# Performance work log

Hardware: AMD Instinct MI355X
Metric: run time of the kernel (lower is better)

## Reference

```python
import jax, jax.numpy as jnp
import numpy as np

B, S, H = 4, 2048, 1024

def setup_inputs() -> dict:
    key = jax.random.key(0)
    ks = jax.random.split(key, 6)
    scale = 1.0 / np.sqrt(H)
    return {
        "query": jax.random.normal(ks[0], (B, S, H), dtype=jnp.float32),
        "key":   jax.random.normal(ks[1], (B, S, H), dtype=jnp.float32),
        "value": jax.random.normal(ks[2], (B, S, H), dtype=jnp.float32),
        "Wq": jax.random.normal(ks[3], (H, H), dtype=jnp.float32) * scale,
        "Wk": jax.random.normal(ks[4], (H, H), dtype=jnp.float32) * scale,
        "Wv": jax.random.normal(ks[5], (H, H), dtype=jnp.float32) * scale,
    }

def reference(query, key, value, Wq, Wk, Wv):
    # nn.Linear(bias=False): y = x @ W.T
    q = jnp.einsum('bsh,oh->bso', query, Wq)
    k = jnp.einsum('bsh,oh->bso', key, Wk)
    v = jnp.einsum('bsh,oh->bso', value, Wv)
    # full QK^T scores [B, Q, K], scaled by sqrt(hidden_size)
    scores = jnp.einsum('bqh,bkh->bqk', q, k) / jnp.sqrt(jnp.asarray(H, q.dtype))
    attn = jax.nn.softmax(scores, axis=2)
    return jnp.einsum('bqk,bkh->bqh', attn, v)
```

## Files before the change

### kernel.cpp

```cpp
#include <hip/hip_runtime.h>
#include <hip/hip_bf16.h>
#include <stdint.h>

#define BATCH 4
#define SLEN  2048
#define HID   1024

typedef __attribute__((ext_vector_type(8))) short bfrag8;
typedef __attribute__((ext_vector_type(4))) float facc4;
typedef __attribute__((ext_vector_type(4))) unsigned short us4;

__device__ __forceinline__ unsigned short f2b(float f) {
  union { float f; unsigned int i; } x; x.f = f;
  unsigned int r = x.i + 0x7FFFu + ((x.i >> 16) & 1u);
  return (unsigned short)(r >> 16);
}

__device__ __forceinline__ void gl_lds16(const void* g, void* l) {
  __builtin_amdgcn_global_load_lds(
      (const __attribute__((address_space(1))) void*)g,
      (__attribute__((address_space(3))) void*)l, 16, 0, 0);
}

__global__ __launch_bounds__(256) void cast_all(
    const float* __restrict__ q, const float* __restrict__ k,
    const float* __restrict__ v, const float* __restrict__ wq,
    const float* __restrict__ wk, const float* __restrict__ wv,
    us4* __restrict__ dst, float* __restrict__ lsum) {
  if (blockIdx.x < 8) {
    float4 z = {0.f, 0.f, 0.f, 0.f};
    ((float4*)lsum)[blockIdx.x * 256 + threadIdx.x] = z;
  }
  const long i = (long)blockIdx.x * 256 + threadIdx.x;
  const long S1 = 2097152, S2 = 4194304, S3 = 6291456,
             S4 = 6553600, S5 = 6815744;
  const float4* src; long off;
  if (i < S2) {
    if (i < S1) { src = (const float4*)q;  off = i; }
    else        { src = (const float4*)k;  off = i - S1; }
  } else if (i < S3) { src = (const float4*)v;  off = i - S2; }
  else if   (i < S4) { src = (const float4*)wq; off = i - S3; }
  else if   (i < S5) { src = (const float4*)wk; off = i - S4; }
  else               { src = (const float4*)wv; off = i - S5; }
  float4 x = src[off];
  us4 o;
  o.x = f2b(x.x); o.y = f2b(x.y); o.z = f2b(x.z); o.w = f2b(x.w);
  dst[i] = o;
}

template <int NT>
__device__ __forceinline__ void core256(
    const unsigned short* __restrict__ A, const unsigned short* __restrict__ B,
    const int lda, const int ldb,
    unsigned short* __restrict__ As, unsigned short* __restrict__ Bs,
    facc4 (&acc)[8][4]) {
  const int tid  = threadIdx.x;
  const int lane = tid & 63;
  const int wave = tid >> 6;
  const int wm = wave >> 2;
  const int wn = wave & 3;
  const int ln = lane & 15;
  const int lq = lane >> 4;
  const int swz = ln & 7;

  const int row0 = tid >> 3;
  const int blk  = (tid & 7) ^ (row0 & 7);
  const unsigned short* pA = A + (long)row0 * lda + blk * 8;
  const unsigned short* pB = B + (long)row0 * ldb + blk * 8;
  const long a64 = 64l * lda, b64 = 64l * ldb;
  unsigned short* dA = As + tid * 8;
  unsigned short* dB = Bs + tid * 8;

#define STG_A(h, b, t) do { const unsigned short* g_ = pA + (h) * (a64 * 2) + (long)(t) * 64; \
    gl_lds16(g_,       dA + (b) * 16384 + (h) * 8192); \
    gl_lds16(g_ + a64, dA + (b) * 16384 + (h) * 8192 + 4096); } while (0)
#define STG_B(h, b, t) do { const unsigned short* g_ = pB + (h) * (b64 * 2) + (long)(t) * 64; \
    gl_lds16(g_,       dB + (b) * 16384 + (h) * 8192); \
    gl_lds16(g_ + b64, dB + (b) * 16384 + (h) * 8192 + 4096); } while (0)

  const int o0 = (lq ^ swz) * 8;
  const int o1 = ((4 + lq) ^ swz) * 8;
  const int aOfs = wm * 8192 + ln * 64;
  const int bOfs = (wn >> 1) * 8192 + ((wn & 1) * 64 + ln) * 64;

#define RD_A4(dst, bufb, mb) do { \
  _Pragma("unroll") for (int m_ = 0; m_ < 4; ++m_) { \
    dst[m_][0] = *(const bfrag8*)(As + (bufb) + aOfs + ((mb) + m_) * 1024 + o0); \
    dst[m_][1] = *(const bfrag8*)(As + (bufb) + aOfs + ((mb) + m_) * 1024 + o1); \
  } } while (0)
#define RD_B2(dst, bufb, nb) do { \
  _Pragma("unroll") for (int n_ = 0; n_ < 2; ++n_) { \
    dst[n_][0] = *(const bfrag8*)(Bs + (bufb) + bOfs + ((nb) + n_) * 1024 + o0); \
    dst[n_][1] = *(const bfrag8*)(Bs + (bufb) + bOfs + ((nb) + n_) * 1024 + o1); \
  } } while (0)

#define MFMAQ(AF, BF, MO, NO) do { \
  _Pragma("unroll") for (int m_ = 0; m_ < 4; ++m_) \
  _Pragma("unroll") for (int n_ = 0; n_ < 2; ++n_) { \
    acc[(MO)+m_][(NO)+n_] = __builtin_amdgcn_mfma_f32_16x16x32_bf16( \
        AF[m_][0], BF[n_][0], acc[(MO)+m_][(NO)+n_], 0, 0, 0); \
    acc[(MO)+m_][(NO)+n_] = __builtin_amdgcn_mfma_f32_16x16x32_bf16( \
        AF[m_][1], BF[n_][1], acc[(MO)+m_][(NO)+n_], 0, 0, 0); \
  } } while (0)

  bfrag8 a0[4][2], a1[4][2], b0[2][2], b1[2][2], a0n[4][2], b0n[2][2];

  STG_B(0, 0, 0); STG_A(0, 0, 0); STG_A(1, 0, 0); STG_B(1, 0, 0);
  STG_B(0, 1, 1); STG_A(0, 1, 1); STG_A(1, 1, 1); STG_B(1, 1, 1);
  asm volatile("s_waitcnt vmcnt(8)" ::: "memory");
  __builtin_amdgcn_s_barrier();
  RD_A4(a0, 0, 0);
  RD_B2(b0, 0, 0);

#pragma unroll
  for (int t = 0; t < NT; ++t) {
    const int bb = (t & 1) * 16384;
    const int nb = bb ^ 16384;

    RD_B2(b1, bb, 2);
    __builtin_amdgcn_s_setprio(1);
    MFMAQ(a0, b0, 0, 0);
    __builtin_amdgcn_s_setprio(0);
    __builtin_amdgcn_s_barrier();

    RD_A4(a1, bb, 4);
    if (t + 2 < NT) STG_B(0, t & 1, t + 2);
    __builtin_amdgcn_s_setprio(1);
    MFMAQ(a0, b1, 0, 2);
    __builtin_amdgcn_s_setprio(0);
    if (t + 2 < NT) asm volatile("s_waitcnt vmcnt(2)" ::: "memory");
    else            asm volatile("s_waitcnt vmcnt(0)" ::: "memory");
    __builtin_amdgcn_s_barrier();

    if (t + 1 < NT) RD_A4(a0n, nb, 0);
    if (t + 2 < NT) STG_A(0, t & 1, t + 2);
    __builtin_amdgcn_s_setprio(1);
    MFMAQ(a1, b1, 4, 2);
    __builtin_amdgcn_s_setprio(0);

    if (t + 1 < NT) RD_B2(b0n, nb, 0);
    if (t + 2 < NT) { STG_A(1, t & 1, t + 2); STG_B(1, t & 1, t + 2); }
    __builtin_amdgcn_s_setprio(1);
    MFMAQ(a1, b0, 4, 0);
    __builtin_amdgcn_s_setprio(0);
    __builtin_amdgcn_s_barrier();

    if (t + 1 < NT) {
#pragma unroll
      for (int m_ = 0; m_ < 4; ++m_) { a0[m_][0] = a0n[m_][0]; a0[m_][1] = a0n[m_][1]; }
#pragma unroll
      for (int n_ = 0; n_ < 2; ++n_) { b0[n_][0] = b0n[n_][0]; b0[n_][1] = b0n[n_][1]; }
    }
  }
#undef MFMAQ
#undef RD_A4
#undef RD_B2
#undef STG_A
#undef STG_B
}

__global__ __launch_bounds__(512, 2) void proj3_256(
    const unsigned short* __restrict__ Xq, const unsigned short* __restrict__ Wqb,
    const unsigned short* __restrict__ Xk, const unsigned short* __restrict__ Wkb,
    const unsigned short* __restrict__ Xv, const unsigned short* __restrict__ Wvb,
    unsigned short* __restrict__ Qb, unsigned short* __restrict__ Kb,
    unsigned short* __restrict__ Vt) {
  extern __shared__ unsigned short smem[];
  unsigned short* As = smem;
  unsigned short* Bs = smem + 32768;

  const int pid = blockIdx.x;
  const int p2  = (pid & 7) * 48 + (pid >> 3);
  const int g   = p2 >> 7;
  const int within = p2 & 127;

  const unsigned short* A; const unsigned short* B; unsigned short* C;
  long bm, bn; int ldc_;
  if (g == 0)      { A = Xq;  B = Wqb; C = Qb; }
  else if (g == 1) { A = Xk;  B = Wkb; C = Kb; }
  else             { A = Wvb; B = Xv;  C = Vt; }
  if (g < 2) { bm = (long)(within >> 2) * 256; bn = (long)(within & 3)  * 256; ldc_ = 1024; }
  else       { bm = (long)(within >> 5) * 256; bn = (long)(within & 31) * 256; ldc_ = 8192; }

  facc4 acc[8][4] = {};
  core256<HID / 64>(A + bm * 1024, B + bn * 1024, 1024, 1024, As, Bs, acc);

  const int lane = threadIdx.x & 63, wave = threadIdx.x >> 6;
  const int wm = wave >> 2, wn = wave & 3;
  const int ln = lane & 15, lq = lane >> 4;
#pragma unroll
  for (int m = 0; m < 8; ++m)
#pragma unroll
    for (int n = 0; n < 4; ++n) {
      const long mm = bm + wm * 128 + m * 16 + lq * 4;
      const long nn = bn + wn * 64 + n * 16 + ln;
#pragma unroll
      for (int r = 0; r < 4; ++r)
        C[(mm + r) * (long)ldc_ + nn] = f2b(acc[m][n][r]);
    }
}

__global__ __launch_bounds__(512, 2) void scores256(
    const unsigned short* __restrict__ Q, const unsigned short* __restrict__ Kb,
    unsigned short* __restrict__ P, float* __restrict__ lsum) {
  extern __shared__ unsigned short smem[];
  unsigned short* As = smem;
  unsigned short* Bs = smem + 32768;

  const long z = blockIdx.z;
  const int pid = blockIdx.y * 8 + blockIdx.x;
  const int p2  = (pid & 7) * 8 + (pid >> 3);
  const long bm = (long)(p2 >> 3) * 256;
  const long bn = (long)(p2 & 7) * 256;

  const long SH = (long)SLEN * HID, SS = (long)SLEN * SLEN;
  facc4 acc[8][4] = {};
  core256<HID / 64>(Q + z * SH + bm * 1024, Kb + z * SH + bn * 1024, 1024, 1024,
                    As, Bs, acc);

  unsigned short* Pz = P + z * SS;
  float* lz = lsum + z * SLEN;
  const int lane = threadIdx.x & 63, wave = threadIdx.x >> 6;
  const int wm = wave >> 2, wn = wave & 3;
  const int ln = lane & 15, lq = lane >> 4;
#pragma unroll
  for (int m = 0; m < 8; ++m) {
#pragma unroll
    for (int r = 0; r < 4; ++r) {
      const long q = bm + wm * 128 + m * 16 + lq * 4 + r;
      float rowsum = 0.f;
#pragma unroll
      for (int n = 0; n < 4; ++n) {
        const long kcol = bn + wn * 64 + n * 16 + ln;
        float e = __expf(acc[m][n][r] * 0.03125f);
        Pz[q * (long)SLEN + kcol] = f2b(e);
        rowsum += e;
      }
      rowsum += __shfl_xor(rowsum, 1, 64);
      rowsum += __shfl_xor(rowsum, 2, 64);
      rowsum += __shfl_xor(rowsum, 4, 64);
      rowsum += __shfl_xor(rowsum, 8, 64);
      if (ln == 0) atomicAdd(&lz[q], rowsum);
    }
  }
}

template <int MODE, typename OutT>
__global__ __launch_bounds__(256) void gemm_nt(
    const unsigned short* __restrict__ A, const unsigned short* __restrict__ B,
    OutT* __restrict__ C, int K, int lda, int ldb, int ldc,
    long aStrideZ, long bStrideZ, long cStrideZ, float alpha,
    float* __restrict__ lsum) {
  A += (long)blockIdx.z * aStrideZ;
  B += (long)blockIdx.z * bStrideZ;
  C += (long)blockIdx.z * cStrideZ;
  const long lz = (long)blockIdx.z * SLEN;

  const int nbm = gridDim.x, nbn = gridDim.y;
  const int nb  = nbm * nbn;
  const int pid = blockIdx.y * nbm + blockIdx.x;
  const int p2  = (pid & 7) * (nb >> 3) + (pid >> 3);
  const int GROUP = 4;
  const int gsize = GROUP * nbn;
  const int gid   = p2 / gsize;
  const int rem   = p2 - gid * gsize;
  const long bm = (long)(gid * GROUP + (rem & (GROUP - 1))) * 128;
  const long bn = (long)(rem >> 2) * 128;

  __shared__ __align__(16) unsigned short As[128 * 64];
  __shared__ __align__(16) unsigned short Bs[128 * 64];

  const int tid  = threadIdx.x;
  const int lane = tid & 63;
  const int wave = tid >> 6;
  const int wr   = (wave >> 1) * 64;
  const int wc   = (wave & 1) * 64;
  const int ln   = lane & 15;
  const int lq   = lane >> 4;
  const int swz  = ln & 7;

  facc4 acc[4][4] = {};

  const unsigned short* ap[4]; const unsigned short* bp[4];
  unsigned short* asd[4]; unsigned short* bsd[4];
#pragma unroll
  for (int j = 0; j < 4; ++j) {
    const int c   = j * 256 + tid;
    const int row = c >> 3;
    const int src = ((c & 7) ^ (row & 7)) * 8;
    ap[j]  = A + (bm + row) * (long)lda + src;
    bp[j]  = B + (bn + row) * (long)ldb + src;
    asd[j] = &As[c * 8];
    bsd[j] = &Bs[c * 8];
  }

  for (int k0 = 0; k0 < K; k0 += 64) {
#pragma unroll
    for (int j = 0; j < 4; ++j) { gl_lds16(ap[j], asd[j]); ap[j] += 64; }
#pragma unroll
    for (int j = 0; j < 4; ++j) { gl_lds16(bp[j], bsd[j]); bp[j] += 64; }
    __syncthreads();

#pragma unroll
    for (int kk = 0; kk < 2; ++kk) {
      bfrag8 af[4], bfr[4];
#pragma unroll
      for (int i = 0; i < 4; ++i)
        af[i] = *(const bfrag8*)&As[(wr + i * 16 + ln) * 64 + ((kk * 4 + lq) ^ swz) * 8];
#pragma unroll
      for (int j = 0; j < 4; ++j)
        bfr[j] = *(const bfrag8*)&Bs[(wc + j * 16 + ln) * 64 + ((kk * 4 + lq) ^ swz) * 8];
#pragma unroll
      for (int i = 0; i < 4; ++i)
#pragma unroll
        for (int j = 0; j < 4; ++j)
          acc[i][j] = __builtin_amdgcn_mfma_f32_16x16x32_bf16(af[i], bfr[j], acc[i][j], 0, 0, 0);
    }
    __syncthreads();
  }

  if constexpr (MODE == 1) {
#pragma unroll
    for (int i = 0; i < 4; ++i) {
#pragma unroll
      for (int r = 0; r < 4; ++r) {
        const long m = bm + wr + i * 16 + lq * 4 + r;
        float rowsum = 0.f;
#pragma unroll
        for (int j = 0; j < 4; ++j) {
          const long n = bn + wc + j * 16 + ln;
          float e = __expf(acc[i][j][r] * alpha);
          C[m * (long)ldc + n] = (OutT)f2b(e);
          rowsum += e;
        }
        rowsum += __shfl_xor(rowsum, 1, 64);
        rowsum += __shfl_xor(rowsum, 2, 64);
        rowsum += __shfl_xor(rowsum, 4, 64);
        rowsum += __shfl_xor(rowsum, 8, 64);
        if (ln == 0) atomicAdd(&lsum[lz + m], rowsum);
      }
    }
  } else {
    float inv[16];
#pragma unroll
    for (int i = 0; i < 4; ++i)
#pragma unroll
      for (int r = 0; r < 4; ++r)
        inv[i * 4 + r] = 1.0f / lsum[lz + bm + wr + i * 16 + lq * 4 + r];
#pragma unroll
    for (int i = 0; i < 4; ++i)
#pragma unroll
      for (int j = 0; j < 4; ++j) {
        const long m = bm + wr + i * 16 + lq * 4;
        const long n = bn + wc + j * 16 + ln;
#pragma unroll
        for (int r = 0; r < 4; ++r)
          ((float*)C)[(m + r) * (long)ldc + n] = acc[i][j][r] * inv[i * 4 + r];
      }
  }
}

extern "C" void kernel_launch(void* const* d_in, const int* in_sizes, int n_in,
                              void* d_out, int out_size, void* d_ws, size_t ws_size,
                              hipStream_t stream) {
  const float* q_in = (const float*)d_in[0];
  const float* k_in = (const float*)d_in[1];
  const float* v_in = (const float*)d_in[2];
  const float* wq   = (const float*)d_in[3];
  const float* wk   = (const float*)d_in[4];
  const float* wv   = (const float*)d_in[5];
  float* out = (float*)d_out;

  const long NXH = (long)BATCH * SLEN * HID;
  const long NW  = (long)HID * HID;
  const long SH  = (long)SLEN * HID;
  const long SS  = (long)SLEN * SLEN;

  unsigned short* ws = (unsigned short*)d_ws;
  unsigned short* Xq  = ws;
  unsigned short* Xk  = Xq  + NXH;
  unsigned short* Xv  = Xk  + NXH;
  unsigned short* Wqb = Xv  + NXH;
  unsigned short* Wkb = Wqb + NW;
  unsigned short* Wvb = Wkb + NW;
  unsigned short* Qb  = Wvb + NW;
  unsigned short* Kb  = Qb  + NXH;
  unsigned short* Vt  = Kb  + NXH;
  float*          lsum = (float*)(Vt + NXH);
  unsigned short* P   = Xq;

  static bool attr_done = false;
  if (!attr_done) {
    hipFuncSetAttribute(reinterpret_cast<const void*>(proj3_256),
                        hipFuncAttributeMaxDynamicSharedMemorySize, 131072);
    hipFuncSetAttribute(reinterpret_cast<const void*>(scores256),
                        hipFuncAttributeMaxDynamicSharedMemorySize, 131072);
    attr_done = true;
  }

  cast_all<<<dim3(27648), dim3(256), 0, stream>>>(q_in, k_in, v_in, wq, wk, wv,
                                                  (us4*)ws, lsum);

  proj3_256<<<dim3(384), dim3(512), 131072, stream>>>(
      Xq, Wqb, Xk, Wkb, Xv, Wvb, Qb, Kb, Vt);

  scores256<<<dim3(8, 8, BATCH), dim3(512), 131072, stream>>>(Qb, Kb, P, lsum);

  gemm_nt<2, float><<<dim3(16, 8, BATCH), dim3(256), 0, stream>>>(
      P, Vt, out, SLEN, SLEN, BATCH * SLEN, HID, SS, SLEN, SH, 1.0f, lsum);
}
```

Before: 288.2 us.

## Restructure GEMM main loop into explicit barrier-fenced phases with staggered staging

Rewrites the projection GEMM's K-loop as a rolled loop over pairs of tiles, hardcoding LDS buffer offsets. Each of the four MFMA quadrants is fenced by barriers, lgkmcnt waits and sched_barriers in a ping-pong style. The A half of the next tile is now staged one phase later and B two tiles ahead, which changes the prologue. The aim is to overlap LDS reads and global-to-LDS loads with the MFMAs more predictably and to cut code size from full unrolling, at the cost of more barriers per iteration.

Result: no change. 283.3 us (-1.7%).

```diff
diff --git a/kernel.cpp b/kernel.cpp
--- a/kernel.cpp
+++ b/kernel.cpp
@@ -103,55 +103,86 @@
         AF[m_][1], BF[n_][1], acc[(MO)+m_][(NO)+n_], 0, 0, 0); \
   } } while (0)
 
-  bfrag8 a0[4][2], a1[4][2], b0[2][2], b1[2][2], a0n[4][2], b0n[2][2];
-
-  STG_B(0, 0, 0); STG_A(0, 0, 0); STG_A(1, 0, 0); STG_B(1, 0, 0);
-  STG_B(0, 1, 1); STG_A(0, 1, 1); STG_A(1, 1, 1); STG_B(1, 1, 1);
-  asm volatile("s_waitcnt vmcnt(8)" ::: "memory");
+#define PH_MID \
+  __builtin_amdgcn_s_barrier(); \
+  asm volatile("s_waitcnt lgkmcnt(0)" ::: "memory"); \
+  __builtin_amdgcn_sched_barrier(0); \
+  __builtin_amdgcn_s_setprio(1)
+#define PH_END \
+  __builtin_amdgcn_s_setprio(0); \
+  __builtin_amdgcn_sched_barrier(0); \
+  __builtin_amdgcn_s_barrier()
+
+  STG_A(0, 0, 0); STG_A(1, 0, 0); STG_B(0, 0, 0); STG_B(1, 0, 0);
+  STG_B(0, 1, 1); STG_B(1, 1, 1);
+  asm volatile("s_waitcnt vmcnt(4)" ::: "memory");
   __builtin_amdgcn_s_barrier();
-  RD_A4(a0, 0, 0);
-  RD_B2(b0, 0, 0);
-
-#pragma unroll
-  for (int t = 0; t < NT; ++t) {
-    const int bb = (t & 1) * 16384;
-    const int nb = bb ^ 16384;
-
-    RD_B2(b1, bb, 2);
-    __builtin_amdgcn_s_setprio(1);
-    MFMAQ(a0, b0, 0, 0);
-    __builtin_amdgcn_s_setprio(0);
-    __builtin_amdgcn_s_barrier();
-
-    RD_A4(a1, bb, 4);
-    if (t + 2 < NT) STG_B(0, t & 1, t + 2);
-    __builtin_amdgcn_s_setprio(1);
-    MFMAQ(a0, b1, 0, 2);
-    __builtin_amdgcn_s_setprio(0);
-    if (t + 2 < NT) asm volatile("s_waitcnt vmcnt(2)" ::: "memory");
-    else            asm volatile("s_waitcnt vmcnt(0)" ::: "memory");
-    __builtin_amdgcn_s_barrier();
-
-    if (t + 1 < NT) RD_A4(a0n, nb, 0);
-    if (t + 2 < NT) STG_A(0, t & 1, t + 2);
-    __builtin_amdgcn_s_setprio(1);
-    MFMAQ(a1, b1, 4, 2);
-    __builtin_amdgcn_s_setprio(0);
-
-    if (t + 1 < NT) RD_B2(b0n, nb, 0);
-    if (t + 2 < NT) { STG_A(1, t & 1, t + 2); STG_B(1, t & 1, t + 2); }
-    __builtin_amdgcn_s_setprio(1);
-    MFMAQ(a1, b0, 4, 0);
-    __builtin_amdgcn_s_setprio(0);
-    __builtin_amdgcn_s_barrier();
-
-    if (t + 1 < NT) {
-#pragma unroll
-      for (int m_ = 0; m_ < 4; ++m_) { a0[m_][0] = a0n[m_][0]; a0[m_][1] = a0n[m_][1]; }
-#pragma unroll
-      for (int n_ = 0; n_ < 2; ++n_) { b0[n_][0] = b0n[n_][0]; b0[n_][1] = b0n[n_][1]; }
-    }
-  }
+
+  constexpr int NI = NT / 2;
+#pragma unroll 1
+  for (int i = 0; i < NI - 1; ++i) {
+    const int O1 = 2 * i + 1, E2 = 2 * i + 2, O2 = 2 * i + 3;
+    {
+      bfrag8 a0[4][2], a1[4][2], b0[2][2], b1[2][2];
+      RD_A4(a0, 0, 0); RD_B2(b0, 0, 0); STG_A(0, 1, O1);
+      PH_MID; MFMAQ(a0, b0, 0, 0); PH_END;
+      RD_B2(b1, 0, 2); STG_A(1, 1, O1);
+      PH_MID; MFMAQ(a0, b1, 0, 2); PH_END;
+      RD_A4(a1, 0, 4); STG_B(0, 0, E2);
+      PH_MID; MFMAQ(a1, b1, 4, 2); PH_END;
+      STG_B(1, 0, E2);
+      PH_MID; MFMAQ(a1, b0, 4, 0);
+      __builtin_amdgcn_s_setprio(0);
+      __builtin_amdgcn_sched_barrier(0);
+      asm volatile("s_waitcnt vmcnt(4)" ::: "memory");
+      __builtin_amdgcn_s_barrier();
+    }
+    {
+      bfrag8 a0[4][2], a1[4][2], b0[2][2], b1[2][2];
+      RD_A4(a0, 16384, 0); RD_B2(b0, 16384, 0); STG_A(0, 0, E2);
+      PH_MID; MFMAQ(a0, b0, 0, 0); PH_END;
+      RD_B2(b1, 16384, 2); STG_A(1, 0, E2);
+      PH_MID; MFMAQ(a0, b1, 0, 2); PH_END;
+      RD_A4(a1, 16384, 4); STG_B(0, 1, O2);
+      PH_MID; MFMAQ(a1, b1, 4, 2); PH_END;
+      STG_B(1, 1, O2);
+      PH_MID; MFMAQ(a1, b0, 4, 0);
+      __builtin_amdgcn_s_setprio(0);
+      __builtin_amdgcn_sched_barrier(0);
+      asm volatile("s_waitcnt vmcnt(4)" ::: "memory");
+      __builtin_amdgcn_s_barrier();
+    }
+  }
+  {
+    const int O1 = NT - 1;
+    {
+      bfrag8 a0[4][2], a1[4][2], b0[2][2], b1[2][2];
+      RD_A4(a0, 0, 0); RD_B2(b0, 0, 0); STG_A(0, 1, O1);
+      PH_MID; MFMAQ(a0, b0, 0, 0); PH_END;
+      RD_B2(b1, 0, 2); STG_A(1, 1, O1);
+      PH_MID; MFMAQ(a0, b1, 0, 2); PH_END;
+      RD_A4(a1, 0, 4);
+      PH_MID; MFMAQ(a1, b1, 4, 2); PH_END;
+      PH_MID; MFMAQ(a1, b0, 4, 0);
+      __builtin_amdgcn_s_setprio(0);
+      __builtin_amdgcn_sched_barrier(0);
+      asm volatile("s_waitcnt vmcnt(0)" ::: "memory");
+      __builtin_amdgcn_s_barrier();
+    }
+    {
+      bfrag8 a0[4][2], a1[4][2], b0[2][2], b1[2][2];
+      RD_A4(a0, 16384, 0); RD_B2(b0, 16384, 0);
+      PH_MID; MFMAQ(a0, b0, 0, 0); PH_END;
+      RD_B2(b1, 16384, 2);
+      PH_MID; MFMAQ(a0, b1, 0, 2); PH_END;
+      RD_A4(a1, 16384, 4);
+      PH_MID; MFMAQ(a1, b1, 4, 2); PH_END;
+      PH_MID; MFMAQ(a1, b0, 4, 0);
+      __builtin_amdgcn_s_setprio(0);
+    }
+  }
+#undef PH_MID
+#undef PH_END
 #undef MFMAQ
 #undef RD_A4
 #undef RD_B2
```
